# Performance work log

Hardware: AMD Instinct MI355X
Metric: run time of the kernel (lower is better)

Reference implementation:

```python
import jax, jax.numpy as jnp
import numpy as np

N = 50000   # nodes
E = 200000  # edges
G = 2048    # graphs in batch
H = 300     # hidden_dim
L = 5       # nlayer
AF, AV = 9, 128   # atom features, vocab per feature
BF, BV = 3, 16    # bond features, vocab per feature


def setup_inputs() -> dict:
    key = jax.random.key(0)
    ks = jax.random.split(key, 10)
    s = 0.05
    batch = jnp.sort(jax.random.randint(ks[0], (N,), 0, G))
    x = jax.random.randint(ks[1], (N, AF), 0, AV)
    edge_index = jax.random.randint(ks[2], (2, E), 0, N)
    edge_attr = jax.random.randint(ks[3], (E, BF), 0, BV)
    atom_emb = jax.random.normal(ks[4], (AF * AV, H), dtype=jnp.float32) * s
    bond_emb = jax.random.normal(ks[5], (BF * BV, H), dtype=jnp.float32) * s
    W1 = jax.random.normal(ks[6], (L, H, 2 * H), dtype=jnp.float32) * s
    b1 = jnp.zeros((L, 2 * H), jnp.float32)
    g1 = jnp.ones((L, 2 * H), jnp.float32)
    be1 = jnp.zeros((L, 2 * H), jnp.float32)
    W2 = jax.random.normal(ks[7], (L, 2 * H, H), dtype=jnp.float32) * s
    b2 = jnp.zeros((L, H), jnp.float32)
    g2 = jnp.ones((L, H), jnp.float32)   # outer BatchNorm gamma
    be2 = jnp.zeros((L, H), jnp.float32)  # outer BatchNorm beta
    return dict(batch=batch, x=x, edge_index=edge_index, edge_attr=edge_attr,
                atom_emb=atom_emb, bond_emb=bond_emb,
                W1=W1, b1=b1, g1=g1, be1=be1, W2=W2, b2=b2, g2=g2, be2=be2)


def _bn(z, g, b):
    # training-mode BatchNorm1d over the node/batch dim
    m = z.mean(0)
    v = z.var(0)
    return (z - m) * jax.lax.rsqrt(v + 1e-5) * g + b


def reference(batch, x, edge_index, edge_attr, atom_emb, bond_emb,
              W1, b1, g1, be1, W2, b2, g2, be2):
    # AtomEncoder / BondEncoder: sum of per-feature embeddings (flat-table gather)
    h = atom_emb[x + jnp.arange(AF) * AV].sum(axis=1)          # [N, H]
    e = bond_emb[edge_attr + jnp.arange(BF) * BV].sum(axis=1)  # [E, H]
    src, dst = edge_index[0], edge_index[1]
    for i in range(L):
        # GINEConv: out = MLP((1+eps)*x + sum_j relu(x_j + e_ij)), eps=0
        msg = jax.nn.relu(h[src] + e)                          # [E, H]
        agg = jax.ops.segment_sum(msg, dst, num_segments=N)    # [N, H]
        z = h + agg
        z = jax.nn.relu(_bn(z @ W1[i] + b1[i], g1[i], be1[i])) # Linear+BN+ReLU
        z = z @ W2[i] + b2[i]                                  # Linear
        z = _bn(z, g2[i], be2[i])                              # outer BatchNorm
        h = z if i == L - 1 else jax.nn.relu(z)                # dropout p=0.0 -> identity
    xpool = jax.ops.segment_sum(h, batch, num_segments=G)     # global_add_pool
    return (h, xpool)
```

## Files before the change

### kernel.cpp

```cpp
#include <hip/hip_runtime.h>

#define N_NODES 50000
#define N_EDGES 200000
#define N_GRAPHS 2048
#define HDIM 300
#define HDIM2 600
#define NLAYER 5
#define K1P 320
#define N1P 640
#define N2P 384

#define MT1 ((N_NODES + 127) / 128)
#define NWG1 (5 * MT1)
#define NWG2 (3 * MT1)

#define NCOMBO 4096

#define SCAN_BLK 1024
#define NSCAN ((N_NODES + SCAN_BLK - 1) / SCAN_BLK)

typedef __attribute__((ext_vector_type(8))) _Float16 f16x8;
typedef __attribute__((ext_vector_type(8))) unsigned short ushort8;
typedef __attribute__((ext_vector_type(4))) float f32x4;

__device__ __forceinline__ unsigned short f2h(float f) {
    _Float16 h = (_Float16)f;
    return __builtin_bit_cast(unsigned short, h);
}
__device__ __forceinline__ float h2f(unsigned short u) {
    _Float16 h = __builtin_bit_cast(_Float16, u);
    return (float)h;
}

__device__ __forceinline__ int lower_bound_i(const int* a, int n, int key) {
    int lo = 0, hi = n;
    while (lo < hi) { int mid = (lo + hi) >> 1; if (a[mid] < key) lo = mid + 1; else hi = mid; }
    return lo;
}

__device__ __forceinline__ int xcd_swz(int orig, int nwg) {
    int q = nwg >> 3, r = nwg & 7;
    int xcd = orig & 7;
    int base = (xcd < r) ? xcd * (q + 1) : r * (q + 1) + (xcd - r) * q;
    return base + (orig >> 3);
}

__global__ void k_init(int* deg, int* fill, float* s1, float* q1, float* s2, float* q2) {
    int i = blockIdx.x * blockDim.x + threadIdx.x;
    if (i < N_NODES) { deg[i] = 0; fill[i] = 0; }
    if (i < N1P)     { s1[i] = 0.f; q1[i] = 0.f; }
    if (i < K1P)     { s2[i] = 0.f; q2[i] = 0.f; }
}

__global__ void k_atom(const int* __restrict__ x, const float* __restrict__ atom_emb,
                       unsigned short* __restrict__ hf) {
    int idx = blockIdx.x * blockDim.x + threadIdx.x;
    if (idx >= N_NODES * K1P) return;
    int n = idx / K1P;
    int c = idx - n * K1P;
    if (c >= HDIM) { hf[idx] = 0; return; }
    const int* xr = x + n * 9;
    float acc = 0.f;
#pragma unroll
    for (int f = 0; f < 9; ++f) {
        int row = xr[f] + f * 128;
        acc += atom_emb[(size_t)row * HDIM + c];
    }
    hf[idx] = f2h(acc);
}

__global__ void k_ecomb(const float* __restrict__ bond_emb, unsigned short* __restrict__ ecomb) {
    int t = blockIdx.x * blockDim.x + threadIdx.x;
    if (t >= NCOMBO * HDIM) return;
    int idx = t / HDIM, c = t - idx * HDIM;
    int a0 = idx & 15, a1 = (idx >> 4) & 15, a2 = idx >> 8;
    float v = bond_emb[(size_t)a0 * HDIM + c]
            + bond_emb[(size_t)(16 + a1) * HDIM + c]
            + bond_emb[(size_t)(32 + a2) * HDIM + c];
    ecomb[t] = f2h(v);
}

__global__ void k_deg(const int* __restrict__ dst, int* deg) {
    int j = blockIdx.x * blockDim.x + threadIdx.x;
    if (j < N_EDGES) atomicAdd(&deg[dst[j]], 1);
}

__global__ void k_scan1(const int* __restrict__ deg, int* __restrict__ part,
                        int* __restrict__ psum) {
    __shared__ int buf[SCAN_BLK];
    int b = blockIdx.x, tid = threadIdx.x;
    int i = b * SCAN_BLK + tid;
    int v = (i < N_NODES) ? deg[i] : 0;
    buf[tid] = v;
    __syncthreads();
    for (int off = 1; off < SCAN_BLK; off <<= 1) {
        int t = (tid >= off) ? buf[tid - off] : 0;
        __syncthreads();
        buf[tid] += t;
        __syncthreads();
    }
    if (i < N_NODES) part[i] = buf[tid];
    if (tid == SCAN_BLK - 1) psum[b] = buf[tid];
}

__global__ void k_scan2(int* __restrict__ psum) {
    __shared__ int buf[64];
    int tid = threadIdx.x;
    int v = (tid < NSCAN) ? psum[tid] : 0;
    buf[tid] = v;
    __syncthreads();
    for (int off = 1; off < 64; off <<= 1) {
        int t = (tid >= off) ? buf[tid - off] : 0;
        __syncthreads();
        buf[tid] += t;
        __syncthreads();
    }
    if (tid < NSCAN) psum[tid] = buf[tid] - v;
}

__global__ void k_scan3(const int* __restrict__ part, const int* __restrict__ psum,
                        int* __restrict__ rowptr) {
    int i = blockIdx.x * blockDim.x + threadIdx.x;
    if (i == 0) rowptr[0] = 0;
    if (i < N_NODES) rowptr[i + 1] = part[i] + psum[i / SCAN_BLK];
}

__global__ void k_fill(const int* __restrict__ src, const int* __restrict__ dst,
                       const int* __restrict__ eattr, const int* __restrict__ rowptr,
                       int* fill, int2* __restrict__ csr_rec) {
    int j = blockIdx.x * blockDim.x + threadIdx.x;
    if (j < N_EDGES) {
        int d = dst[j];
        int p = atomicAdd(&fill[d], 1);
        int pos = rowptr[d] + p;
        int combo = eattr[j * 3 + 0] | (eattr[j * 3 + 1] << 4) | (eattr[j * 3 + 2] << 8);
        csr_rec[pos] = make_int2(src[j], combo);
    }
}

__global__ void k_wconv(const float* __restrict__ W, unsigned short* __restrict__ Bt,
                        int K, int NC, int KPAD, int NPAD) {
    int idx = blockIdx.x * blockDim.x + threadIdx.x;
    int tot = NLAYER * NPAD * KPAD;
    if (idx >= tot) return;
    int l = idx / (NPAD * KPAD);
    int rem = idx - l * NPAD * KPAD;
    int n = rem / KPAD;
    int k = rem - n * KPAD;
    float v = (k < K && n < NC) ? W[((size_t)l * K + k) * NC + n] : 0.f;
    Bt[idx] = f2h(v);
}

template <bool BN>
__global__ __launch_bounds__(256) void k_msg(const unsigned short* __restrict__ hsrc,
                                             const float* __restrict__ sc,
                                             const float* __restrict__ sh,
                                             const int* __restrict__ rowptr,
                                             const int2* __restrict__ csr_rec,
                                             const unsigned short* __restrict__ ecomb,
                                             unsigned short* __restrict__ zin) {
    int wid = threadIdx.x >> 6, lane = threadIdx.x & 63;
    int n = blockIdx.x * 4 + wid;
    if (n >= N_NODES) return;

    float scv[5], shv[5], acc[5];
#pragma unroll
    for (int q = 0; q < 5; ++q) {
        int c = lane + 64 * q;
        scv[q] = 0.f; shv[q] = 0.f; acc[q] = 0.f;
        if (c < HDIM) {
            if (BN) { scv[q] = sc[c]; shv[q] = sh[c]; }
            float v = h2f(hsrc[(size_t)n * K1P + c]);
            if (BN) v = fmaxf(v * scv[q] + shv[q], 0.f);
            acc[q] = v;
        }
    }

    int beg = rowptr[n], end = rowptr[n + 1];
    int p = beg;
    for (; p + 2 <= end; p += 2) {
        int2 r0 = csr_rec[p];
        int2 r1 = csr_rec[p + 1];
        const unsigned short* h0 = hsrc + (size_t)r0.x * K1P;
        const unsigned short* h1 = hsrc + (size_t)r1.x * K1P;
        const unsigned short* e0 = ecomb + (size_t)r0.y * HDIM;
        const unsigned short* e1 = ecomb + (size_t)r1.y * HDIM;
#pragma unroll
        for (int q = 0; q < 5; ++q) {
            int c = lane + 64 * q;
            if (c < HDIM) {
                float v0 = h2f(h0[c]);
                float v1 = h2f(h1[c]);
                if (BN) {
                    v0 = fmaxf(v0 * scv[q] + shv[q], 0.f);
                    v1 = fmaxf(v1 * scv[q] + shv[q], 0.f);
                }
                float m0 = v0 + h2f(e0[c]);
                float m1 = v1 + h2f(e1[c]);
                acc[q] += fmaxf(m0, 0.f) + fmaxf(m1, 0.f);
            }
        }
    }
    if (p < end) {
        int2 r0 = csr_rec[p];
        const unsigned short* h0 = hsrc + (size_t)r0.x * K1P;
        const unsigned short* e0 = ecomb + (size_t)r0.y * HDIM;
#pragma unroll
        for (int q = 0; q < 5; ++q) {
            int c = lane + 64 * q;
            if (c < HDIM) {
                float v0 = h2f(h0[c]);
                if (BN) v0 = fmaxf(v0 * scv[q] + shv[q], 0.f);
                float m0 = v0 + h2f(e0[c]);
                acc[q] += fmaxf(m0, 0.f);
            }
        }
    }
    unsigned short* zr = zin + (size_t)n * K1P;
#pragma unroll
    for (int q = 0; q < 5; ++q) {
        int c = lane + 64 * q;
        if (c < HDIM) zr[c] = f2h(acc[q]);
    }
}

__global__ __launch_bounds__(256, 4) void k_mfma1(const unsigned short* __restrict__ A,
                                                  const unsigned short* __restrict__ Bt,
                                                  const float* __restrict__ bias,
                                                  unsigned short* __restrict__ Ch,
                                                  float* __restrict__ gsum,
                                                  float* __restrict__ gssq) {
    __shared__ unsigned short tA[2][128 * 32];
    __shared__ unsigned short tB[2][128 * 32];
    __shared__ float csum[128], cssq[128];

    const int tid = threadIdx.x;
    const int lane = tid & 63, wid = tid >> 6;
    const int wm = wid >> 1, wn = wid & 1;
    const int wgid = xcd_swz(blockIdx.x, NWG1);
    const int n0 = (wgid % 5) * 128, m0 = (wgid / 5) * 128;
    const int fr = lane & 15, fq = lane >> 4;

    f32x4 acc[4][4] = {};
    const int arow = lane >> 2;
    const int achk = (lane & 3) * 8;
    const int sk = achk ^ ((arow & 3) << 3);
    const int swr = (fr & 3) << 3;
    constexpr int NT = K1P / 32;

    auto stage = [&](int buf, int kt) {
        const int k0 = kt * 32;
#pragma unroll
        for (int i = 0; i < 2; ++i) {
            int grp = i * 4 + wid;
            int grow = m0 + grp * 16 + arow;
            if (grow >= N_NODES) grow = N_NODES - 1;
            const unsigned short* ga = A + (size_t)grow * K1P + k0 + sk;
            __builtin_amdgcn_global_load_lds((const __attribute__((address_space(1))) void*)ga,
                                             (__attribute__((address_space(3))) void*)&tA[buf][grp * 512],
                                             16, 0, 0);
            int gn = n0 + grp * 16 + arow;
            const unsigned short* gb = Bt + (size_t)gn * K1P + k0 + sk;
            __builtin_amdgcn_global_load_lds((const __attribute__((address_space(1))) void*)gb,
                                             (__attribute__((address_space(3))) void*)&tB[buf][grp * 512],
                                             16, 0, 0);
        }
    };

    stage(0, 0);
    __syncthreads();

    int cur = 0;
    for (int kt = 0; kt < NT; ++kt) {
        if (kt + 1 < NT) stage(cur ^ 1, kt + 1);

        f16x8 af[4], bfr[4];
#pragma unroll
        for (int t = 0; t < 4; ++t) {
            af[t]  = *(const f16x8*)&tA[cur][(wm * 64 + t * 16 + fr) * 32 + (fq * 8 ^ swr)];
            bfr[t] = *(const f16x8*)&tB[cur][(wn * 64 + t * 16 + fr) * 32 + (fq * 8 ^ swr)];
        }
#pragma unroll
        for (int mt = 0; mt < 4; ++mt)
#pragma unroll
            for (int nt = 0; nt < 4; ++nt)
                acc[mt][nt] = __builtin_amdgcn_mfma_f32_16x16x32_f16(af[mt], bfr[nt], acc[mt][nt], 0, 0, 0);

        __syncthreads();
        cur ^= 1;
    }

    float bv[4];
#pragma unroll
    for (int nt = 0; nt < 4; ++nt) {
        int col = n0 + wn * 64 + nt * 16 + fr;
        bv[nt] = (col < HDIM2) ? bias[col] : 0.f;
    }
    if (tid < 128) { csum[tid] = 0.f; cssq[tid] = 0.f; }
    __syncthreads();

    float colS[4] = {0.f, 0.f, 0.f, 0.f};
    float colQ[4] = {0.f, 0.f, 0.f, 0.f};
#pragma unroll
    for (int mt = 0; mt < 4; ++mt) {
#pragma unroll
        for (int r = 0; r < 4; ++r) {
            int row = m0 + wm * 64 + mt * 16 + fq * 4 + r;
            bool rok = row < N_NODES;
#pragma unroll
            for (int nt = 0; nt < 4; ++nt) {
                int col = n0 + wn * 64 + nt * 16 + fr;
                if (rok && col < HDIM2) {
                    float v = acc[mt][nt][r] + bv[nt];
                    Ch[(size_t)row * N1P + col] = f2h(v);
                    colS[nt] += v;
                    colQ[nt] += v * v;
                }
            }
        }
    }
#pragma unroll
    for (int nt = 0; nt < 4; ++nt) {
        int c = wn * 64 + nt * 16 + fr;
        atomicAdd(&csum[c], colS[nt]);
        atomicAdd(&cssq[c], colQ[nt]);
    }
    __syncthreads();
    if (tid < 128) {
        int col = n0 + tid;
        if (col < HDIM2) {
            atomicAdd(&gsum[col], csum[tid]);
            atomicAdd(&gssq[col], cssq[tid]);
        }
    }
}

__global__ __launch_bounds__(256, 3) void k_mfma2(const unsigned short* __restrict__ z1,
                                                  const unsigned short* __restrict__ Bt,
                                                  const float* __restrict__ bias,
                                                  const unsigned short* __restrict__ scaleAh,
                                                  const unsigned short* __restrict__ shiftAh,
                                                  unsigned short* __restrict__ Ch,
                                                  float* __restrict__ gsum,
                                                  float* __restrict__ gssq) {
    __shared__ unsigned short tA[2][128 * 32];
    __shared__ unsigned short tB[2][128 * 32];
    __shared__ float csum[128], cssq[128];

    const int tid = threadIdx.x;
    const int lane = tid & 63, wid = tid >> 6;
    const int wm = wid >> 1, wn = wid & 1;
    const int wgid = xcd_swz(blockIdx.x, NWG2);
    const int n0 = (wgid % 3) * 128, m0 = (wgid / 3) * 128;
    const int fr = lane & 15, fq = lane >> 4;

    f32x4 acc[4][4] = {};
    const int arow = lane >> 2;
    const int achk = (lane & 3) * 8;
    const int sk = achk ^ ((arow & 3) << 3);
    const int swr = (fr & 3) << 3;
    constexpr int NT = N1P / 32;

    auto stage = [&](int buf, int kt) {
        const int k0 = kt * 32;
#pragma unroll
        for (int i = 0; i < 2; ++i) {
            int grp = i * 4 + wid;
            int grow = m0 + grp * 16 + arow;
            if (grow >= N_NODES) grow = N_NODES - 1;
            const unsigned short* ga = z1 + (size_t)grow * N1P + k0 + sk;
            __builtin_amdgcn_global_load_lds((const __attribute__((address_space(1))) void*)ga,
                                             (__attribute__((address_space(3))) void*)&tA[buf][grp * 512],
                                             16, 0, 0);
            int gn = n0 + grp * 16 + arow;
            const unsigned short* gb = Bt + (size_t)gn * N1P + k0 + sk;
            __builtin_amdgcn_global_load_lds((const __attribute__((address_space(1))) void*)gb,
                                             (__attribute__((address_space(3))) void*)&tB[buf][grp * 512],
                                             16, 0, 0);
        }
    };

    stage(0, 0);
    __syncthreads();

    int cur = 0;
    for (int kt = 0; kt < NT; ++kt) {
        if (kt + 1 < NT) stage(cur ^ 1, kt + 1);

        const int kc = kt * 32 + fq * 8;
        f16x8 sa = *(const f16x8*)&scaleAh[kc];
        f16x8 sb = *(const f16x8*)&shiftAh[kc];
        f16x8 af[4], bfr[4];
#pragma unroll
        for (int t = 0; t < 4; ++t) {
            f16x8 z = *(const f16x8*)&tA[cur][(wm * 64 + t * 16 + fr) * 32 + (fq * 8 ^ swr)];
            f16x8 r;
#pragma unroll
            for (int j = 0; j < 8; ++j) {
                _Float16 v = z[j] * sa[j] + sb[j];
                r[j] = (v > (_Float16)0) ? v : (_Float16)0;
            }
            af[t] = r;
            bfr[t] = *(const f16x8*)&tB[cur][(wn * 64 + t * 16 + fr) * 32 + (fq * 8 ^ swr)];
        }
#pragma unroll
        for (int mt = 0; mt < 4; ++mt)
#pragma unroll
            for (int nt = 0; nt < 4; ++nt)
                acc[mt][nt] = __builtin_amdgcn_mfma_f32_16x16x32_f16(af[mt], bfr[nt], acc[mt][nt], 0, 0, 0);

        __syncthreads();
        cur ^= 1;
    }

    float bv[4];
#pragma unroll
    for (int nt = 0; nt < 4; ++nt) {
        int col = n0 + wn * 64 + nt * 16 + fr;
        bv[nt] = (col < HDIM) ? bias[col] : 0.f;
    }
    if (tid < 128) { csum[tid] = 0.f; cssq[tid] = 0.f; }
    __syncthreads();

    float colS[4] = {0.f, 0.f, 0.f, 0.f};
    float colQ[4] = {0.f, 0.f, 0.f, 0.f};
#pragma unroll
    for (int mt = 0; mt < 4; ++mt) {
#pragma unroll
        for (int r = 0; r < 4; ++r) {
            int row = m0 + wm * 64 + mt * 16 + fq * 4 + r;
            bool rok = row < N_NODES;
#pragma unroll
            for (int nt = 0; nt < 4; ++nt) {
                int col = n0 + wn * 64 + nt * 16 + fr;
                if (rok && col < HDIM) {
                    float v = acc[mt][nt][r] + bv[nt];
                    Ch[(size_t)row * K1P + col] = f2h(v);
                    colS[nt] += v;
                    colQ[nt] += v * v;
                }
            }
        }
    }
#pragma unroll
    for (int nt = 0; nt < 4; ++nt) {
        int c = wn * 64 + nt * 16 + fr;
        atomicAdd(&csum[c], colS[nt]);
        atomicAdd(&cssq[c], colQ[nt]);
    }
    __syncthreads();
    if (tid < 128) {
        int col = n0 + tid;
        if (col < HDIM) {
            atomicAdd(&gsum[col], csum[tid]);
            atomicAdd(&gssq[col], cssq[tid]);
        }
    }
}

__global__ void k_fin(const float* __restrict__ gsum, const float* __restrict__ gssq,
                      const float* __restrict__ gamma, const float* __restrict__ beta,
                      int C, int CPAD, float* __restrict__ scale, float* __restrict__ shift,
                      unsigned short* scaleh, unsigned short* shifth,
                      float* zs, float* zq, int CZ) {
    int i = blockIdx.x * blockDim.x + threadIdx.x;
    if (i < CPAD) {
        float sc = 0.f, sh = 0.f;
        if (i < C) {
            float m = gsum[i] * (1.f / (float)N_NODES);
            float v = gssq[i] * (1.f / (float)N_NODES) - m * m;
            float rs = rsqrtf(v + 1e-5f);
            sc = rs * gamma[i];
            sh = beta[i] - m * sc;
        }
        scale[i] = sc;
        shift[i] = sh;
        if (scaleh) { scaleh[i] = f2h(sc); shifth[i] = f2h(sh); }
    }
    if (i < CZ) { zs[i] = 0.f; zq[i] = 0.f; }
}

__global__ void k_normf(const unsigned short* __restrict__ z2,
                        const float* __restrict__ scale, const float* __restrict__ shift,
                        float* __restrict__ out_h) {
    int idx = blockIdx.x * blockDim.x + threadIdx.x;
    if (idx >= N_NODES * (K1P / 4)) return;
    int row = idx / (K1P / 4);
    int c = (idx % (K1P / 4)) * 4;
    if (c >= HDIM) return;
    const unsigned short* zr = z2 + (size_t)row * K1P + c;
    float4 o;
    o.x = h2f(zr[0]) * scale[c + 0] + shift[c + 0];
    o.y = h2f(zr[1]) * scale[c + 1] + shift[c + 1];
    o.z = h2f(zr[2]) * scale[c + 2] + shift[c + 2];
    o.w = h2f(zr[3]) * scale[c + 3] + shift[c + 3];
    *(float4*)(out_h + (size_t)row * HDIM + c) = o;
}

__global__ __launch_bounds__(128) void k_pool(const float* __restrict__ hfin,
                                              const int* __restrict__ batch,
                                              float* __restrict__ xpool) {
    int g = blockIdx.x;
    int t = threadIdx.x;
    int start = lower_bound_i(batch, N_NODES, g);
    int end   = lower_bound_i(batch, N_NODES, g + 1);
    int cols[3] = { t, t + 128, t + 256 };
    float acc[3] = {0.f, 0.f, 0.f};
    for (int n = start; n < end; ++n) {
        const float* hr = hfin + (size_t)n * HDIM;
#pragma unroll
        for (int q = 0; q < 3; ++q)
            if (cols[q] < HDIM) acc[q] += hr[cols[q]];
    }
#pragma unroll
    for (int q = 0; q < 3; ++q)
        if (cols[q] < HDIM) xpool[(size_t)g * HDIM + cols[q]] = acc[q];
}

extern "C" void kernel_launch(void* const* d_in, const int* in_sizes, int n_in,
                              void* d_out, int out_size, void* d_ws, size_t ws_size,
                              hipStream_t stream) {
    const int*   batch    = (const int*)d_in[0];
    const int*   x        = (const int*)d_in[1];
    const int*   eidx     = (const int*)d_in[2];
    const int*   eattr    = (const int*)d_in[3];
    const float* atom_emb = (const float*)d_in[4];
    const float* bond_emb = (const float*)d_in[5];
    const float* W1 = (const float*)d_in[6];
    const float* b1 = (const float*)d_in[7];
    const float* g1 = (const float*)d_in[8];
    const float* be1 = (const float*)d_in[9];
    const float* W2 = (const float*)d_in[10];
    const float* b2 = (const float*)d_in[11];
    const float* g2 = (const float*)d_in[12];
    const float* be2 = (const float*)d_in[13];

    const int* src = eidx;
    const int* dst = eidx + N_EDGES;

    float* out_h    = (float*)d_out;
    float* out_pool = (float*)d_out + (size_t)N_NODES * HDIM;

    char* ws = (char*)d_ws;
    size_t off = 0;
    auto alloc = [&](size_t bytes) -> void* {
        void* p = ws + off;
        off += (bytes + 255) & ~(size_t)255;
        return p;
    };
    unsigned short* hf    = (unsigned short*)alloc((size_t)N_NODES * K1P * 2);
    unsigned short* zin   = (unsigned short*)alloc((size_t)N_NODES * K1P * 2);
    unsigned short* z1    = (unsigned short*)alloc((size_t)N_NODES * N1P * 2);
    unsigned short* z2    = (unsigned short*)alloc((size_t)N_NODES * K1P * 2);
    unsigned short* W1t   = (unsigned short*)alloc((size_t)NLAYER * N1P * K1P * 2);
    unsigned short* W2t   = (unsigned short*)alloc((size_t)NLAYER * N2P * N1P * 2);
    unsigned short* ecomb = (unsigned short*)alloc((size_t)NCOMBO * HDIM * 2);
    int* rowptr  = (int*)alloc((N_NODES + 1) * sizeof(int));
    int* deg     = (int*)alloc(N_NODES * sizeof(int));
    int* fill    = (int*)alloc(N_NODES * sizeof(int));
    int* part    = (int*)alloc(N_NODES * sizeof(int));
    int* psum    = (int*)alloc(64 * sizeof(int));
    int2* csr_rec = (int2*)alloc((size_t)N_EDGES * sizeof(int2));
    float* s1     = (float*)alloc(N1P * sizeof(float));
    float* q1     = (float*)alloc(N1P * sizeof(float));
    float* scale1 = (float*)alloc(N1P * sizeof(float));
    float* shift1 = (float*)alloc(N1P * sizeof(float));
    unsigned short* scale1h = (unsigned short*)alloc(N1P * sizeof(short));
    unsigned short* shift1h = (unsigned short*)alloc(N1P * sizeof(short));
    float* s2     = (float*)alloc(K1P * sizeof(float));
    float* q2     = (float*)alloc(K1P * sizeof(float));
    float* scale2 = (float*)alloc(K1P * sizeof(float));
    float* shift2 = (float*)alloc(K1P * sizeof(float));

    k_init<<<(N_NODES + 255) / 256, 256, 0, stream>>>(deg, fill, s1, q1, s2, q2);
    k_atom<<<(N_NODES * K1P + 255) / 256, 256, 0, stream>>>(x, atom_emb, hf);
    k_ecomb<<<(NCOMBO * HDIM + 255) / 256, 256, 0, stream>>>(bond_emb, ecomb);
    k_deg<<<(N_EDGES + 255) / 256, 256, 0, stream>>>(dst, deg);
    k_scan1<<<NSCAN, SCAN_BLK, 0, stream>>>(deg, part, psum);
    k_scan2<<<1, 64, 0, stream>>>(psum);
    k_scan3<<<(N_NODES + 255) / 256, 256, 0, stream>>>(part, psum, rowptr);
    k_fill<<<(N_EDGES + 255) / 256, 256, 0, stream>>>(src, dst, eattr, rowptr,
                                                      fill, csr_rec);
    {
        int tot1 = NLAYER * N1P * K1P;
        k_wconv<<<(tot1 + 255) / 256, 256, 0, stream>>>(W1, W1t, HDIM, HDIM2, K1P, N1P);
        int tot2 = NLAYER * N2P * N1P;
        k_wconv<<<(tot2 + 255) / 256, 256, 0, stream>>>(W2, W2t, HDIM2, HDIM, N1P, N2P);
    }

    int msg_grid = (N_NODES + 3) / 4;
    for (int l = 0; l < NLAYER; ++l) {
        if (l == 0) {
            k_msg<false><<<msg_grid, 256, 0, stream>>>(hf, nullptr, nullptr,
                                                       rowptr, csr_rec, ecomb, zin);
        } else {
            k_msg<true><<<msg_grid, 256, 0, stream>>>(z2, scale2, shift2,
                                                      rowptr, csr_rec, ecomb, zin);
        }

        k_mfma1<<<NWG1, 256, 0, stream>>>(
            zin, W1t + (size_t)l * N1P * K1P, b1 + (size_t)l * HDIM2, z1, s1, q1);

        k_fin<<<3, 256, 0, stream>>>(s1, q1, g1 + (size_t)l * HDIM2, be1 + (size_t)l * HDIM2,
                                     HDIM2, N1P, scale1, shift1, scale1h, shift1h,
                                     s2, q2, K1P);

        k_mfma2<<<NWG2, 256, 0, stream>>>(
            z1, W2t + (size_t)l * N2P * N1P, b2 + (size_t)l * HDIM,
            scale1h, shift1h, z2, s2, q2);

        k_fin<<<3, 256, 0, stream>>>(s2, q2, g2 + (size_t)l * HDIM, be2 + (size_t)l * HDIM,
                                     HDIM, K1P, scale2, shift2, nullptr, nullptr,
                                     s1, q1, N1P);
    }

    k_normf<<<(N_NODES * (K1P / 4) + 255) / 256, 256, 0, stream>>>(
        z2, scale2, shift2, out_h);

    k_pool<<<N_GRAPHS, 128, 0, stream>>>(out_h, batch, out_pool);
}
```

Baseline: 1.061 ms.

## Load MFMA operands directly from global memory into registers, dropping LDS staging

Both GEMM kernels stop staging A/B tiles through shared memory with global_load_lds and barriers. Each wave now loads its own fragments straight from global memory into registers, using a two-deep register double buffer. Occupancy hints drop to 2 waves-per-EU to make room for the extra registers. This removes LDS traffic and __syncthreads, but operands are no longer shared across waves, so global/L2 traffic rises (about 2x duplicate reads) and loads are uncoalesced per-lane 16-byte rows.

```diff
diff --git a/kernel.cpp b/kernel.cpp
--- a/kernel.cpp
+++ b/kernel.cpp
@@ -224,14 +224,12 @@
     }
 }
 
-__global__ __launch_bounds__(256, 4) void k_mfma1(const unsigned short* __restrict__ A,
+__global__ __launch_bounds__(256, 2) void k_mfma1(const unsigned short* __restrict__ A,
                                                   const unsigned short* __restrict__ Bt,
                                                   const float* __restrict__ bias,
                                                   unsigned short* __restrict__ Ch,
                                                   float* __restrict__ gsum,
                                                   float* __restrict__ gssq) {
-    __shared__ unsigned short tA[2][128 * 32];
-    __shared__ unsigned short tB[2][128 * 32];
     __shared__ float csum[128], cssq[128];
 
     const int tid = threadIdx.x;
@@ -242,52 +240,43 @@
     const int fr = lane & 15, fq = lane >> 4;
 
     f32x4 acc[4][4] = {};
-    const int arow = lane >> 2;
-    const int achk = (lane & 3) * 8;
-    const int sk = achk ^ ((arow & 3) << 3);
-    const int swr = (fr & 3) << 3;
     constexpr int NT = K1P / 32;
 
-    auto stage = [&](int buf, int kt) {
-        const int k0 = kt * 32;
-#pragma unroll
-        for (int i = 0; i < 2; ++i) {
-            int grp = i * 4 + wid;
-            int grow = m0 + grp * 16 + arow;
-            if (grow >= N_NODES) grow = N_NODES - 1;
-            const unsigned short* ga = A + (size_t)grow * K1P + k0 + sk;
-            __builtin_amdgcn_global_load_lds((const __attribute__((address_space(1))) void*)ga,
-                                             (__attribute__((address_space(3))) void*)&tA[buf][grp * 512],
-                                             16, 0, 0);
-            int gn = n0 + grp * 16 + arow;
-            const unsigned short* gb = Bt + (size_t)gn * K1P + k0 + sk;
-            __builtin_amdgcn_global_load_lds((const __attribute__((address_space(1))) void*)gb,
-                                             (__attribute__((address_space(3))) void*)&tB[buf][grp * 512],
-                                             16, 0, 0);
-        }
-    };
-
-    stage(0, 0);
-    __syncthreads();
-
-    int cur = 0;
-    for (int kt = 0; kt < NT; ++kt) {
-        if (kt + 1 < NT) stage(cur ^ 1, kt + 1);
-
-        f16x8 af[4], bfr[4];
-#pragma unroll
-        for (int t = 0; t < 4; ++t) {
-            af[t]  = *(const f16x8*)&tA[cur][(wm * 64 + t * 16 + fr) * 32 + (fq * 8 ^ swr)];
-            bfr[t] = *(const f16x8*)&tB[cur][(wn * 64 + t * 16 + fr) * 32 + (fq * 8 ^ swr)];
+    const unsigned short* pa[4];
+    const unsigned short* pb[4];
+#pragma unroll
+    for (int t = 0; t < 4; ++t) {
+        int r = m0 + wm * 64 + t * 16 + fr; if (r >= N_NODES) r = N_NODES - 1;
+        pa[t] = A + (size_t)r * K1P + fq * 8;
+        int c = n0 + wn * 64 + t * 16 + fr;
+        pb[t] = Bt + (size_t)c * K1P + fq * 8;
+    }
+
+    f16x8 ca[4], cb[4], na[4], nb[4];
+#pragma unroll
+    for (int t = 0; t < 4; ++t) { ca[t] = *(const f16x8*)pa[t]; cb[t] = *(const f16x8*)pb[t]; }
+
+    for (int kt = 0; kt < NT; kt += 2) {
+        {
+            const int ko = (kt + 1) * 32;
+#pragma unroll
+            for (int t = 0; t < 4; ++t) { na[t] = *(const f16x8*)(pa[t] + ko); nb[t] = *(const f16x8*)(pb[t] + ko); }
         }
 #pragma unroll
         for (int mt = 0; mt < 4; ++mt)
 #pragma unroll
             for (int nt = 0; nt < 4; ++nt)
-                acc[mt][nt] = __builtin_amdgcn_mfma_f32_16x16x32_f16(af[mt], bfr[nt], acc[mt][nt], 0, 0, 0);
-
-        __syncthreads();
-        cur ^= 1;
+                acc[mt][nt] = __builtin_amdgcn_mfma_f32_16x16x32_f16(ca[mt], cb[nt], acc[mt][nt], 0, 0, 0);
+        if (kt + 2 < NT) {
+            const int ko = (kt + 2) * 32;
+#pragma unroll
+            for (int t = 0; t < 4; ++t) { ca[t] = *(const f16x8*)(pa[t] + ko); cb[t] = *(const f16x8*)(pb[t] + ko); }
+        }
+#pragma unroll
+        for (int mt = 0; mt < 4; ++mt)
+#pragma unroll
+            for (int nt = 0; nt < 4; ++nt)
+                acc[mt][nt] = __builtin_amdgcn_mfma_f32_16x16x32_f16(na[mt], nb[nt], acc[mt][nt], 0, 0, 0);
     }
 
     float bv[4];
@@ -335,7 +324,7 @@
     }
 }
 
-__global__ __launch_bounds__(256, 3) void k_mfma2(const unsigned short* __restrict__ z1,
+__global__ __launch_bounds__(256, 2) void k_mfma2(const unsigned short* __restrict__ z1,
                                                   const unsigned short* __restrict__ Bt,
                                                   const float* __restrict__ bias,
                                                   const unsigned short* __restrict__ scaleAh,
@@ -343,8 +332,6 @@
                                                   unsigned short* __restrict__ Ch,
                                                   float* __restrict__ gsum,
                                                   float* __restrict__ gssq) {
-    __shared__ unsigned short tA[2][128 * 32];
-    __shared__ unsigned short tB[2][128 * 32];
     __shared__ float csum[128], cssq[128];
 
     const int tid = threadIdx.x;
@@ -355,62 +342,67 @@
     const int fr = lane & 15, fq = lane >> 4;
 
     f32x4 acc[4][4] = {};
-    const int arow = lane >> 2;
-    const int achk = (lane & 3) * 8;
-    const int sk = achk ^ ((arow & 3) << 3);
-    const int swr = (fr & 3) << 3;
     constexpr int NT = N1P / 32;
 
-    auto stage = [&](int buf, int kt) {
-        const int k0 = kt * 32;
-#pragma unroll
-        for (int i = 0; i < 2; ++i) {
-            int grp = i * 4 + wid;
-            int grow = m0 + grp * 16 + arow;
-            if (grow >= N_NODES) grow = N_NODES - 1;
-            const unsigned short* ga = z1 + (size_t)grow * N1P + k0 + sk;
-            __builtin_amdgcn_global_load_lds((const __attribute__((address_space(1))) void*)ga,
-                                             (__attribute__((address_space(3))) void*)&tA[buf][grp * 512],
-                                             16, 0, 0);
-            int gn = n0 + grp * 16 + arow;
-            const unsigned short* gb = Bt + (size_t)gn * N1P + k0 + sk;
-            __builtin_amdgcn_global_load_lds((const __attribute__((address_space(1))) void*)gb,
-                                             (__attribute__((address_space(3))) void*)&tB[buf][grp * 512],
-                                             16, 0, 0);
-        }
-    };
-
-    stage(0, 0);
-    __syncthreads();
-
-    int cur = 0;
-    for (int kt = 0; kt < NT; ++kt) {
-        if (kt + 1 < NT) stage(cur ^ 1, kt + 1);
-
-        const int kc = kt * 32 + fq * 8;
+    const unsigned short* pa[4];
+    const unsigned short* pb[4];
+#pragma unroll
+    for (int t = 0; t < 4; ++t) {
+        int r = m0 + wm * 64 + t * 16 + fr; if (r >= N_NODES) r = N_NODES - 1;
+        pa[t] = z1 + (size_t)r * N1P + fq * 8;
+        int c = n0 + wn * 64 + t * 16 + fr;
+        pb[t] = Bt + (size_t)c * N1P + fq * 8;
+    }
+
+    auto xform = [&](f16x8 z, int kc) -> f16x8 {
         f16x8 sa = *(const f16x8*)&scaleAh[kc];
         f16x8 sb = *(const f16x8*)&shiftAh[kc];
-        f16x8 af[4], bfr[4];
-#pragma unroll
-        for (int t = 0; t < 4; ++t) {
-            f16x8 z = *(const f16x8*)&tA[cur][(wm * 64 + t * 16 + fr) * 32 + (fq * 8 ^ swr)];
-            f16x8 r;
-#pragma unroll
-            for (int j = 0; j < 8; ++j) {
-                _Float16 v = z[j] * sa[j] + sb[j];
-                r[j] = (v > (_Float16)0) ? v : (_Float16)0;
-            }
-            af[t] = r;
-            bfr[t] = *(const f16x8*)&tB[cur][(wn * 64 + t * 16 + fr) * 32 + (fq * 8 ^ swr)];
-        }
-#pragma unroll
-        for (int mt = 0; mt < 4; ++mt)
-#pragma unroll
-            for (int nt = 0; nt < 4; ++nt)
-                acc[mt][nt] = __builtin_amdgcn_mfma_f32_16x16x32_f16(af[mt], bfr[nt], acc[mt][nt], 0, 0, 0);
-
-        __syncthreads();
-        cur ^= 1;
+        f16x8 r;
+#pragma unroll
+        for (int j = 0; j < 8; ++j) {
+            _Float16 v = z[j] * sa[j] + sb[j];
+            r[j] = (v > (_Float16)0) ? v : (_Float16)0;
+        }
+        return r;
+    };
+
+    f16x8 ca[4], cb[4], na[4], nb[4];
+#pragma unroll
+    for (int t = 0; t < 4; ++t) { ca[t] = *(const f16x8*)pa[t]; cb[t] = *(const f16x8*)pb[t]; }
+
+    for (int kt = 0; kt < NT; kt += 2) {
+        {
+            const int ko = (kt + 1) * 32;
+#pragma unroll
+            for (int t = 0; t < 4; ++t) { na[t] = *(const f16x8*)(pa[t] + ko); nb[t] = *(const f16x8*)(pb[t] + ko); }
+        }
+        {
+            const int kc = kt * 32 + fq * 8;
+            f16x8 af[4];
+#pragma unroll
+            for (int t = 0; t < 4; ++t) af[t] = xform(ca[t], kc);
+#pragma unroll
+            for (int mt = 0; mt < 4; ++mt)
+#pragma unroll
+                for (int nt = 0; nt < 4; ++nt)
+                    acc[mt][nt] = __builtin_amdgcn_mfma_f32_16x16x32_f16(af[mt], cb[nt], acc[mt][nt], 0, 0, 0);
+        }
+        if (kt + 2 < NT) {
+            const int ko = (kt + 2) * 32;
+#pragma unroll
+            for (int t = 0; t < 4; ++t) { ca[t] = *(const f16x8*)(pa[t] + ko); cb[t] = *(const f16x8*)(pb[t] + ko); }
+        }
+        {
+            const int kc = (kt + 1) * 32 + fq * 8;
+            f16x8 af[4];
+#pragma unroll
+            for (int t = 0; t < 4; ++t) af[t] = xform(na[t], kc);
+#pragma unroll
+            for (int mt = 0; mt < 4; ++mt)
+#pragma unroll
+                for (int nt = 0; nt < 4; ++nt)
+                    acc[mt][nt] = __builtin_amdgcn_mfma_f32_16x16x32_f16(af[mt], nb[nt], acc[mt][nt], 0, 0, 0);
+        }
     }
 
     float bv[4];
```

New measurement: 1.708 ms. +61.0%, slower.

## Use single-wave 64x64 GEMM tiles with triple-buffered LDS and shuffle-reduced BN stats

Applied to the files above, without the earlier changes.

Both MFMA GEMM kernels switch from 256-thread 128x128 workgroups to single-wavefront 64x64 tiles. A three-stage LDS ring with explicit vmcnt waits replaces the double buffer and its per-iteration __syncthreads. Column BatchNorm statistics are now reduced with cross-lane shuffles and global atomics instead of LDS atomics. The LDS XOR swizzle is dropped, which risks bank conflicts on fragment reads, and the smaller tiles lower operand reuse while doubling the global atomics on the statistics buffers.

```diff
diff --git a/kernel.cpp b/kernel.cpp
--- a/kernel.cpp
+++ b/kernel.cpp
@@ -10,9 +10,9 @@
 #define N1P 640
 #define N2P 384
 
-#define MT1 ((N_NODES + 127) / 128)
-#define NWG1 (5 * MT1)
-#define NWG2 (3 * MT1)
+#define MT64 ((N_NODES + 63) / 64)
+#define NWG1 (10 * MT64)
+#define NWG2 (5 * MT64)
 
 #define NCOMBO 4096
 
@@ -224,61 +224,60 @@
     }
 }
 
-__global__ __launch_bounds__(256, 4) void k_mfma1(const unsigned short* __restrict__ A,
-                                                  const unsigned short* __restrict__ Bt,
-                                                  const float* __restrict__ bias,
-                                                  unsigned short* __restrict__ Ch,
-                                                  float* __restrict__ gsum,
-                                                  float* __restrict__ gssq) {
-    __shared__ unsigned short tA[2][128 * 32];
-    __shared__ unsigned short tB[2][128 * 32];
-    __shared__ float csum[128], cssq[128];
-
-    const int tid = threadIdx.x;
-    const int lane = tid & 63, wid = tid >> 6;
-    const int wm = wid >> 1, wn = wid & 1;
+__global__ __launch_bounds__(64) void k_mfma1(const unsigned short* __restrict__ A,
+                                              const unsigned short* __restrict__ Bt,
+                                              const float* __restrict__ bias,
+                                              unsigned short* __restrict__ Ch,
+                                              float* __restrict__ gsum,
+                                              float* __restrict__ gssq) {
+    __shared__ unsigned short tA[3][64 * 32];
+    __shared__ unsigned short tB[3][64 * 32];
+
+    const int lane = threadIdx.x;
     const int wgid = xcd_swz(blockIdx.x, NWG1);
-    const int n0 = (wgid % 5) * 128, m0 = (wgid / 5) * 128;
+    const int n0 = (wgid % 10) * 64, m0 = (wgid / 10) * 64;
     const int fr = lane & 15, fq = lane >> 4;
 
     f32x4 acc[4][4] = {};
-    const int arow = lane >> 2;
-    const int achk = (lane & 3) * 8;
-    const int sk = achk ^ ((arow & 3) << 3);
-    const int swr = (fr & 3) << 3;
+    const int srow = lane >> 2;
+    const int schk = (lane & 3) * 8;
     constexpr int NT = K1P / 32;
 
     auto stage = [&](int buf, int kt) {
         const int k0 = kt * 32;
 #pragma unroll
-        for (int i = 0; i < 2; ++i) {
-            int grp = i * 4 + wid;
-            int grow = m0 + grp * 16 + arow;
+        for (int i = 0; i < 4; ++i) {
+            int grow = m0 + i * 16 + srow;
             if (grow >= N_NODES) grow = N_NODES - 1;
-            const unsigned short* ga = A + (size_t)grow * K1P + k0 + sk;
+            const unsigned short* ga = A + (size_t)grow * K1P + k0 + schk;
             __builtin_amdgcn_global_load_lds((const __attribute__((address_space(1))) void*)ga,
-                                             (__attribute__((address_space(3))) void*)&tA[buf][grp * 512],
+                                             (__attribute__((address_space(3))) void*)&tA[buf][i * 512],
                                              16, 0, 0);
-            int gn = n0 + grp * 16 + arow;
-            const unsigned short* gb = Bt + (size_t)gn * K1P + k0 + sk;
+            int gn = n0 + i * 16 + srow;
+            const unsigned short* gb = Bt + (size_t)gn * K1P + k0 + schk;
             __builtin_amdgcn_global_load_lds((const __attribute__((address_space(1))) void*)gb,
-                                             (__attribute__((address_space(3))) void*)&tB[buf][grp * 512],
+                                             (__attribute__((address_space(3))) void*)&tB[buf][i * 512],
                                              16, 0, 0);
         }
     };
 
     stage(0, 0);
-    __syncthreads();
+    stage(1, 1);
 
     int cur = 0;
     for (int kt = 0; kt < NT; ++kt) {
-        if (kt + 1 < NT) stage(cur ^ 1, kt + 1);
+        if (kt + 1 < NT) asm volatile("s_waitcnt vmcnt(8)" ::: "memory");
+        else             asm volatile("s_waitcnt vmcnt(0)" ::: "memory");
+        if (kt + 2 < NT) {
+            int nb = cur + 2; if (nb >= 3) nb -= 3;
+            stage(nb, kt + 2);
+        }
 
         f16x8 af[4], bfr[4];
 #pragma unroll
         for (int t = 0; t < 4; ++t) {
-            af[t]  = *(const f16x8*)&tA[cur][(wm * 64 + t * 16 + fr) * 32 + (fq * 8 ^ swr)];
-            bfr[t] = *(const f16x8*)&tB[cur][(wn * 64 + t * 16 + fr) * 32 + (fq * 8 ^ swr)];
+            af[t]  = *(const f16x8*)&tA[cur][(t * 16 + fr) * 32 + fq * 8];
+            bfr[t] = *(const f16x8*)&tB[cur][(t * 16 + fr) * 32 + fq * 8];
         }
 #pragma unroll
         for (int mt = 0; mt < 4; ++mt)
@@ -286,30 +285,26 @@
             for (int nt = 0; nt < 4; ++nt)
                 acc[mt][nt] = __builtin_amdgcn_mfma_f32_16x16x32_f16(af[mt], bfr[nt], acc[mt][nt], 0, 0, 0);
 
-        __syncthreads();
-        cur ^= 1;
+        cur = (cur == 2) ? 0 : cur + 1;
     }
 
     float bv[4];
 #pragma unroll
     for (int nt = 0; nt < 4; ++nt) {
-        int col = n0 + wn * 64 + nt * 16 + fr;
+        int col = n0 + nt * 16 + fr;
         bv[nt] = (col < HDIM2) ? bias[col] : 0.f;
     }
-    if (tid < 128) { csum[tid] = 0.f; cssq[tid] = 0.f; }
-    __syncthreads();
-
     float colS[4] = {0.f, 0.f, 0.f, 0.f};
     float colQ[4] = {0.f, 0.f, 0.f, 0.f};
 #pragma unroll
     for (int mt = 0; mt < 4; ++mt) {
 #pragma unroll
         for (int r = 0; r < 4; ++r) {
-            int row = m0 + wm * 64 + mt * 16 + fq * 4 + r;
+            int row = m0 + mt * 16 + fq * 4 + r;
             bool rok = row < N_NODES;
 #pragma unroll
             for (int nt = 0; nt < 4; ++nt) {
-                int col = n0 + wn * 64 + nt * 16 + fr;
+                int col = n0 + nt * 16 + fr;
                 if (rok && col < HDIM2) {
                     float v = acc[mt][nt][r] + bv[nt];
                     Ch[(size_t)row * N1P + col] = f2h(v);
@@ -321,71 +316,73 @@
     }
 #pragma unroll
     for (int nt = 0; nt < 4; ++nt) {
-        int c = wn * 64 + nt * 16 + fr;
-        atomicAdd(&csum[c], colS[nt]);
-        atomicAdd(&cssq[c], colQ[nt]);
-    }
-    __syncthreads();
-    if (tid < 128) {
-        int col = n0 + tid;
-        if (col < HDIM2) {
-            atomicAdd(&gsum[col], csum[tid]);
-            atomicAdd(&gssq[col], cssq[tid]);
-        }
-    }
-}
-
-__global__ __launch_bounds__(256, 3) void k_mfma2(const unsigned short* __restrict__ z1,
-                                                  const unsigned short* __restrict__ Bt,
-                                                  const float* __restrict__ bias,
-                                                  const unsigned short* __restrict__ scaleAh,
-                                                  const unsigned short* __restrict__ shiftAh,
-                                                  unsigned short* __restrict__ Ch,
-                                                  float* __restrict__ gsum,
-                                                  float* __restrict__ gssq) {
-    __shared__ unsigned short tA[2][128 * 32];
-    __shared__ unsigned short tB[2][128 * 32];
-    __shared__ float csum[128], cssq[128];
-
-    const int tid = threadIdx.x;
-    const int lane = tid & 63, wid = tid >> 6;
-    const int wm = wid >> 1, wn = wid & 1;
+        colS[nt] += __shfl_xor(colS[nt], 16);
+        colS[nt] += __shfl_xor(colS[nt], 32);
+        colQ[nt] += __shfl_xor(colQ[nt], 16);
+        colQ[nt] += __shfl_xor(colQ[nt], 32);
+    }
+    if (lane < 16) {
+#pragma unroll
+        for (int nt = 0; nt < 4; ++nt) {
+            int col = n0 + nt * 16 + fr;
+            if (col < HDIM2) {
+                atomicAdd(&gsum[col], colS[nt]);
+                atomicAdd(&gssq[col], colQ[nt]);
+            }
+        }
+    }
+}
+
+__global__ __launch_bounds__(64) void k_mfma2(const unsigned short* __restrict__ z1,
+                                              const unsigned short* __restrict__ Bt,
+                                              const float* __restrict__ bias,
+                                              const unsigned short* __restrict__ scaleAh,
+                                              const unsigned short* __restrict__ shiftAh,
+                                              unsigned short* __restrict__ Ch,
+                                              float* __restrict__ gsum,
+                                              float* __restrict__ gssq) {
+    __shared__ unsigned short tA[3][64 * 32];
+    __shared__ unsigned short tB[3][64 * 32];
+
+    const int lane = threadIdx.x;
     const int wgid = xcd_swz(blockIdx.x, NWG2);
-    const int n0 = (wgid % 3) * 128, m0 = (wgid / 3) * 128;
+    const int n0 = (wgid % 5) * 64, m0 = (wgid / 5) * 64;
     const int fr = lane & 15, fq = lane >> 4;
 
     f32x4 acc[4][4] = {};
-    const int arow = lane >> 2;
-    const int achk = (lane & 3) * 8;
-    const int sk = achk ^ ((arow & 3) << 3);
-    const int swr = (fr & 3) << 3;
+    const int srow = lane >> 2;
+    const int schk = (lane & 3) * 8;
     constexpr int NT = N1P / 32;
 
     auto stage = [&](int buf, int kt) {
         const int k0 = kt * 32;
 #pragma unroll
-        for (int i = 0; i < 2; ++i) {
-            int grp = i * 4 + wid;
-            int grow = m0 + grp * 16 + arow;
+        for (int i = 0; i < 4; ++i) {
+            int grow = m0 + i * 16 + srow;
             if (grow >= N_NODES) grow = N_NODES - 1;
-            const unsigned short* ga = z1 + (size_t)grow * N1P + k0 + sk;
+            const unsigned short* ga = z1 + (size_t)grow * N1P + k0 + schk;
             __builtin_amdgcn_global_load_lds((const __attribute__((address_space(1))) void*)ga,
-                                             (__attribute__((address_space(3))) void*)&tA[buf][grp * 512],
+                                             (__attribute__((address_space(3))) void*)&tA[buf][i * 512],
                                              16, 0, 0);
-            int gn = n0 + grp * 16 + arow;
-            const unsigned short* gb = Bt + (size_t)gn * N1P + k0 + sk;
+            int gn = n0 + i * 16 + srow;
+            const unsigned short* gb = Bt + (size_t)gn * N1P + k0 + schk;
             __builtin_amdgcn_global_load_lds((const __attribute__((address_space(1))) void*)gb,
-                                             (__attribute__((address_space(3))) void*)&tB[buf][grp * 512],
+                                             (__attribute__((address_space(3))) void*)&tB[buf][i * 512],
                                              16, 0, 0);
         }
     };
 
     stage(0, 0);
-    __syncthreads();
+    stage(1, 1);
 
     int cur = 0;
     for (int kt = 0; kt < NT; ++kt) {
-        if (kt + 1 < NT) stage(cur ^ 1, kt + 1);
+        if (kt + 1 < NT) asm volatile("s_waitcnt vmcnt(8)" ::: "memory");
+        else             asm volatile("s_waitcnt vmcnt(0)" ::: "memory");
+        if (kt + 2 < NT) {
+            int nb = cur + 2; if (nb >= 3) nb -= 3;
+            stage(nb, kt + 2);
+        }
 
         const int kc = kt * 32 + fq * 8;
         f16x8 sa = *(const f16x8*)&scaleAh[kc];
@@ -393,7 +390,7 @@
         f16x8 af[4], bfr[4];
 #pragma unroll
         for (int t = 0; t < 4; ++t) {
-            f16x8 z = *(const f16x8*)&tA[cur][(wm * 64 + t * 16 + fr) * 32 + (fq * 8 ^ swr)];
+            f16x8 z = *(const f16x8*)&tA[cur][(t * 16 + fr) * 32 + fq * 8];
             f16x8 r;
 #pragma unroll
             for (int j = 0; j < 8; ++j) {
@@ -401,7 +398,7 @@
                 r[j] = (v > (_Float16)0) ? v : (_Float16)0;
             }
             af[t] = r;
-            bfr[t] = *(const f16x8*)&tB[cur][(wn * 64 + t * 16 + fr) * 32 + (fq * 8 ^ swr)];
+            bfr[t] = *(const f16x8*)&tB[cur][(t * 16 + fr) * 32 + fq * 8];
         }
 #pragma unroll
         for (int mt = 0; mt < 4; ++mt)
@@ -409,30 +406,26 @@
             for (int nt = 0; nt < 4; ++nt)
                 acc[mt][nt] = __builtin_amdgcn_mfma_f32_16x16x32_f16(af[mt], bfr[nt], acc[mt][nt], 0, 0, 0);
 
-        __syncthreads();
-        cur ^= 1;
+        cur = (cur == 2) ? 0 : cur + 1;
     }
 
     float bv[4];
 #pragma unroll
     for (int nt = 0; nt < 4; ++nt) {
-        int col = n0 + wn * 64 + nt * 16 + fr;
+        int col = n0 + nt * 16 + fr;
         bv[nt] = (col < HDIM) ? bias[col] : 0.f;
     }
-    if (tid < 128) { csum[tid] = 0.f; cssq[tid] = 0.f; }
-    __syncthreads();
-
     float colS[4] = {0.f, 0.f, 0.f, 0.f};
     float colQ[4] = {0.f, 0.f, 0.f, 0.f};
 #pragma unroll
     for (int mt = 0; mt < 4; ++mt) {
 #pragma unroll
         for (int r = 0; r < 4; ++r) {
-            int row = m0 + wm * 64 + mt * 16 + fq * 4 + r;
+            int row = m0 + mt * 16 + fq * 4 + r;
             bool rok = row < N_NODES;
 #pragma unroll
             for (int nt = 0; nt < 4; ++nt) {
-                int col = n0 + wn * 64 + nt * 16 + fr;
+                int col = n0 + nt * 16 + fr;
                 if (rok && col < HDIM) {
                     float v = acc[mt][nt][r] + bv[nt];
                     Ch[(size_t)row * K1P + col] = f2h(v);
@@ -444,16 +437,19 @@
     }
 #pragma unroll
     for (int nt = 0; nt < 4; ++nt) {
-        int c = wn * 64 + nt * 16 + fr;
-        atomicAdd(&csum[c], colS[nt]);
-        atomicAdd(&cssq[c], colQ[nt]);
-    }
-    __syncthreads();
-    if (tid < 128) {
-        int col = n0 + tid;
-        if (col < HDIM) {
-            atomicAdd(&gsum[col], csum[tid]);
-            atomicAdd(&gssq[col], cssq[tid]);
+        colS[nt] += __shfl_xor(colS[nt], 16);
+        colS[nt] += __shfl_xor(colS[nt], 32);
+        colQ[nt] += __shfl_xor(colQ[nt], 16);
+        colQ[nt] += __shfl_xor(colQ[nt], 32);
+    }
+    if (lane < 16) {
+#pragma unroll
+        for (int nt = 0; nt < 4; ++nt) {
+            int col = n0 + nt * 16 + fr;
+            if (col < HDIM) {
+                atomicAdd(&gsum[col], colS[nt]);
+                atomicAdd(&gssq[col], colQ[nt]);
+            }
         }
     }
 }
@@ -598,14 +594,14 @@
                                                       rowptr, csr_rec, ecomb, zin);
         }
 
-        k_mfma1<<<NWG1, 256, 0, stream>>>(
+        k_mfma1<<<NWG1, 64, 0, stream>>>(
             zin, W1t + (size_t)l * N1P * K1P, b1 + (size_t)l * HDIM2, z1, s1, q1);
 
         k_fin<<<3, 256, 0, stream>>>(s1, q1, g1 + (size_t)l * HDIM2, be1 + (size_t)l * HDIM2,
                                      HDIM2, N1P, scale1, shift1, scale1h, shift1h,
                                      s2, q2, K1P);
 
-        k_mfma2<<<NWG2, 256, 0, stream>>>(
+        k_mfma2<<<NWG2, 64, 0, stream>>>(
             z1, W2t + (size_t)l * N2P * N1P, b2 + (size_t)l * HDIM,
             scale1h, shift1h, z2, s2, q2);
 
```

New measurement: 1.271 ms. 19.8% more time.
